# Kernel tuning notes

Hardware: AMD Instinct MI355X
Metric: run time of the kernel (lower is better)

The kernel has to match this reference:

```python
import jax, jax.numpy as jnp
import numpy as np

B, P, D_IN = 128, 4096, 4   # frames, points/frame, xyz+time
NG = 16                      # number of trajectory groups
H1, H2, H3 = 64, 128, 512    # PointNet shared-MLP widths


def _init_mlp(key, dims):
    ks = jax.random.split(key, len(dims) - 1)
    params = []
    for k, (di, do) in zip(ks, zip(dims[:-1], dims[1:])):
        W = jax.random.normal(k, (di, do), dtype=jnp.float32) * (1.0 / np.sqrt(di))
        b = jnp.zeros((do,), dtype=jnp.float32)
        params.append((W, b))
    return params


def setup_inputs() -> dict:
    key = jax.random.key(0)
    k_pc, k_t, k_idx, k_g, k_l = jax.random.split(key, 5)
    pc = jax.random.normal(k_pc, (B, 3, P), dtype=jnp.float32)
    traj_time_batch = jax.random.uniform(k_t, (B, 1), dtype=jnp.float32)
    traj_inbatch_index = jnp.sort(jax.random.randint(k_idx, (B,), 0, NG)).astype(jnp.int32)
    (Wg1, bg1), (Wg2, bg2), (Wg3, bg3) = _init_mlp(k_g, [D_IN, H1, H2, H3])
    (Wl1, bl1), (Wl2, bl2), (Wl3, bl3) = _init_mlp(k_l, [D_IN, H1, H2, H3])
    return dict(pc=pc, traj_time_batch=traj_time_batch, traj_inbatch_index=traj_inbatch_index,
                Wg1=Wg1, bg1=bg1, Wg2=Wg2, bg2=bg2, Wg3=Wg3, bg3=bg3,
                Wl1=Wl1, bl1=bl1, Wl2=Wl2, bl2=bl2, Wl3=Wl3, bl3=bl3)


def _mlp(x, layers):
    # pointwise shared MLP: x [..., P, d_in] -> [..., P, d_out]
    for W, b in layers:
        x = jax.nn.relu(x @ W + b)
    return x


def reference(pc, traj_time_batch, traj_inbatch_index,
              Wg1, bg1, Wg2, bg2, Wg3, bg3,
              Wl1, bl1, Wl2, bl2, Wl3, bl3):
    b, _, p = pc.shape
    # append time channel: [B,3,P] + [B,1,P] -> [B,4,P]
    t = jnp.broadcast_to(traj_time_batch[..., None], (b, 1, p))
    feat = jnp.concatenate([pc, t], axis=1)
    x = jnp.swapaxes(feat, 1, 2)  # [B,P,4] points-last layout for pointwise MLP

    # global branch: shared MLP on every point, then max over all points of each trajectory group
    hg = _mlp(x, [(Wg1, bg1), (Wg2, bg2), (Wg3, bg3)])           # [B,P,H3]
    seg = jnp.repeat(traj_inbatch_index, p)                       # [B*P]
    gmax = jax.ops.segment_max(hg.reshape(b * p, -1), seg, num_segments=NG)  # [NG,H3]
    global_feat = gmax[traj_inbatch_index]                        # [B,H3] broadcast back per frame

    # local branch: per-frame PointNet encode (shared MLP + max over points)
    hl = _mlp(x, [(Wl1, bl1), (Wl2, bl2), (Wl3, bl3)])            # [B,P,H3]
    local_feat = hl.max(axis=1)                                   # [B,H3]

    z = jnp.concatenate([global_feat, local_feat], axis=1)        # [B,2*H3]
    input_features_vis = pc                                       # original pc (last dim == 4096, no slice)
    return (z, input_features_vis)
```

## Files before the change

kernel.cpp:

```cpp
#include <hip/hip_runtime.h>
#include <hip/hip_bf16.h>

#define NB   128
#define NP   4096
#define NGRP 16
#define C3   512

typedef __bf16 bf16x8 __attribute__((ext_vector_type(8)));
typedef __bf16 bf16x4 __attribute__((ext_vector_type(4)));
typedef float  f32x4  __attribute__((ext_vector_type(4)));

#define WS_W1F_G 0
#define WS_W1F_L 4096
#define WS_W2F_G 8192
#define WS_W2F_L 24576
#define WS_W3F_G 40960
#define WS_W3F_L 172032
#define WS_GMAX  303104

__global__ __launch_bounds__(256) void prep_kernel(
    const float* __restrict__ Wg1, const float* __restrict__ Wg2, const float* __restrict__ Wg3,
    const float* __restrict__ Wl1, const float* __restrict__ Wl2, const float* __restrict__ Wl3,
    const float* __restrict__ pc, float* __restrict__ out, char* __restrict__ ws) {
    const int t = blockIdx.x, tid = threadIdx.x;
    if (t >= 37) {
        const f32x4* src = (const f32x4*)pc;
        f32x4* dst = (f32x4*)(out + NB * 2 * C3);
        int base = (t - 37) * 1024 + tid;
        #pragma unroll
        for (int j = 0; j < 4; ++j) dst[base + j * 256] = src[base + j * 256];
        return;
    }
    if (t == 36) {
        float* gmax = (float*)(ws + WS_GMAX);
        #pragma unroll
        for (int k = 0; k < 32; ++k) gmax[k * 256 + tid] = 0.0f;
        int c = tid >> 6, lane = tid & 63;
        int ch = c * 16 + (lane & 15);
        int kb = (lane >> 4) * 8;
        bf16x8 pg, pl;
        #pragma unroll
        for (int j = 0; j < 8; ++j) {
            int k = kb + j;
            pg[j] = (k < 4) ? (__bf16)Wg1[k * 64 + ch] : (__bf16)0.0f;
            pl[j] = (k < 4) ? (__bf16)Wl1[k * 64 + ch] : (__bf16)0.0f;
        }
        *(bf16x8*)((__bf16*)(ws + WS_W1F_G) + c * 512 + lane * 8) = pg;
        *(bf16x8*)((__bf16*)(ws + WS_W1F_L) + c * 512 + lane * 8) = pl;
        return;
    }
    __shared__ float tile[64][65];
    const float* src; __bf16* dst; int cBase, mMul, srcStride;
    if (t < 32) {
        int branch = t >> 4, rem = t & 15;
        int tk = rem >> 3, tc = rem & 7;
        src = (branch ? Wl3 : Wg3) + (size_t)(tk * 64) * 512 + tc * 64;
        dst = (__bf16*)(ws + (branch ? WS_W3F_L : WS_W3F_G));
        cBase = tc * 16 + tk * 2; mMul = 4; srcStride = 512;
    } else {
        int u = t - 32; int branch = u >> 1, tc = u & 1;
        src = (branch ? Wl2 : Wg2) + tc * 64;
        dst = (__bf16*)(ws + (branch ? WS_W2F_L : WS_W2F_G));
        cBase = tc * 8; mMul = 2; srcStride = 128;
    }
    {
        int r0 = tid >> 6, cl = tid & 63;
        #pragma unroll
        for (int p = 0; p < 16; ++p)
            tile[p * 4 + r0][cl] = src[(size_t)(p * 4 + r0) * srcStride + cl];
    }
    __syncthreads();
    int lane = tid & 63, l15 = lane & 15, q = lane >> 4;
    #pragma unroll
    for (int cc = 0; cc < 2; ++cc) {
        int pair = (tid >> 6) * 2 + cc;
        int mi = pair >> 1, ks = pair & 1;
        bf16x8 pk;
        #pragma unroll
        for (int j = 0; j < 8; ++j) pk[j] = (__bf16)tile[ks * 32 + q * 8 + j][mi * 16 + l15];
        *(bf16x8*)(dst + (cBase + mi * mMul + ks) * 512 + lane * 8) = pk;
    }
}

__global__ __launch_bounds__(512, 2) void main_kernel(
    const float* __restrict__ pc, const float* __restrict__ tt, const int* __restrict__ idx,
    const float* __restrict__ bg1, const float* __restrict__ bg2, const float* __restrict__ bg3,
    const float* __restrict__ bl1, const float* __restrict__ bl2, const float* __restrict__ bl3,
    float* __restrict__ out, char* __restrict__ ws) {
    __shared__ __align__(16) char smem[102912];
    __bf16* h2f = (__bf16*)smem;
    __bf16* w2f = (__bf16*)(smem + 65536);
    __bf16* h1s = (__bf16*)(smem + 81920);
    float*  b2s = (float*)(smem + 102400);

    const int tid = threadIdx.x, lane = tid & 63, wave = tid >> 6;
    const int quad = lane >> 4, l15 = lane & 15;
    const int branch = blockIdx.y, frame = blockIdx.x;

    const __bf16* w1g = (const __bf16*)(ws + (branch ? WS_W1F_L : WS_W1F_G));
    const __bf16* w2g = (const __bf16*)(ws + (branch ? WS_W2F_L : WS_W2F_G));
    const __bf16* w3g = (const __bf16*)(ws + (branch ? WS_W3F_L : WS_W3F_G));
    const float* b1 = branch ? bl1 : bg1;
    const float* b2 = branch ? bl2 : bg2;
    const float* b3 = branch ? bl3 : bg3;

    for (int i = tid; i < 1024; i += 512) ((f32x4*)w2f)[i] = ((const f32x4*)w2g)[i];
    if (tid < 128) b2s[tid] = b2[tid];

    bf16x8 a1[4];
    #pragma unroll
    for (int mi = 0; mi < 4; ++mi) a1[mi] = *(const bf16x8*)(w1g + mi * 512 + lane * 8);
    bf16x8 aw[4][4];
    #pragma unroll
    for (int mi = 0; mi < 4; ++mi)
        #pragma unroll
        for (int ks = 0; ks < 4; ++ks)
            aw[mi][ks] = *(const bf16x8*)(w3g + (wave * 16 + mi * 4 + ks) * 512 + lane * 8);

    float b1r[4][4];
    #pragma unroll
    for (int mi = 0; mi < 4; ++mi)
        #pragma unroll
        for (int r = 0; r < 4; ++r) b1r[mi][r] = b1[mi * 16 + quad * 4 + r];

    const float tval = tt[frame];
    const f32x4 zf = {0.0f, 0.0f, 0.0f, 0.0f};
    f32x4 runmax[4];
    #pragma unroll
    for (int mi = 0; mi < 4; ++mi) runmax[mi] = (f32x4){-1e30f, -1e30f, -1e30f, -1e30f};

    const float* pcx = pc + (size_t)frame * 3 * NP;
    __bf16* hs = h1s + wave * 1280;
    const int pw = wave * 16 + l15;

    float xx = pcx[pw], xy = pcx[NP + pw], xz = pcx[2 * NP + pw];

    __syncthreads();

    {
        bf16x8 xb;
        #pragma unroll
        for (int j = 0; j < 8; ++j) xb[j] = (__bf16)0.0f;
        if (quad == 0) { xb[0] = (__bf16)xx; xb[1] = (__bf16)xy; xb[2] = (__bf16)xz; xb[3] = (__bf16)tval; }
        #pragma unroll
        for (int mi = 0; mi < 4; ++mi) {
            f32x4 c = __builtin_amdgcn_mfma_f32_16x16x32_bf16(a1[mi], xb, zf, 0, 0, 0);
            bf16x4 pk;
            #pragma unroll
            for (int r = 0; r < 4; ++r) pk[r] = (__bf16)fmaxf(c[r] + b1r[mi][r], 0.0f);
            *(bf16x4*)(hs + l15 * 80 + mi * 16 + quad * 4) = pk;
        }
        bf16x8 hbf0 = *(const bf16x8*)(hs + l15 * 80 + quad * 8);
        bf16x8 hbf1 = *(const bf16x8*)(hs + l15 * 80 + 32 + quad * 8);
        #pragma unroll
        for (int mi = 0; mi < 8; ++mi) {
            bf16x8 a20 = *(const bf16x8*)(w2f + (mi * 2) * 512 + lane * 8);
            bf16x8 a21 = *(const bf16x8*)(w2f + (mi * 2 + 1) * 512 + lane * 8);
            f32x4 c = __builtin_amdgcn_mfma_f32_16x16x32_bf16(a20, hbf0, zf, 0, 0, 0);
            c = __builtin_amdgcn_mfma_f32_16x16x32_bf16(a21, hbf1, c, 0, 0, 0);
            f32x4 bb = *(const f32x4*)(b2s + mi * 16 + quad * 4);
            bf16x4 pk;
            #pragma unroll
            for (int r = 0; r < 4; ++r) pk[r] = (__bf16)fmaxf(c[r] + bb[r], 0.0f);
            const int c0 = mi * 16 + quad * 4;
            *(bf16x4*)(h2f + ((wave * 4 + (c0 >> 5)) * 4 + ((c0 >> 3) & 3)) * 128 + l15 * 8 + (c0 & 7)) = pk;
        }
    }

    for (int m = 0; m < 32; ++m) {
        __syncthreads();
        const __bf16* hb = h2f + (m & 1) * 16384;
        __bf16* hbn = h2f + ((m + 1) & 1) * 16384;
        const bool more = (m < 31);
        float nx = 0.f, ny = 0.f, nz = 0.f;
        if (more) {
            const int p = (m + 1) * 128 + pw;
            nx = pcx[p]; ny = pcx[NP + p]; nz = pcx[2 * NP + p];
        }
        bf16x8 hbf0, hbf1;
        bf16x8 bh0[4], bh1[4];
        #pragma unroll
        for (int ks = 0; ks < 4; ++ks) bh0[ks] = *(const bf16x8*)(hb + ks * 512 + lane * 8);
        #pragma unroll
        for (int ni = 0; ni < 8; ++ni) {
            bf16x8* cur = (ni & 1) ? bh1 : bh0;
            bf16x8* nxt = (ni & 1) ? bh0 : bh1;
            if (ni < 7) {
                #pragma unroll
                for (int ks = 0; ks < 4; ++ks)
                    nxt[ks] = *(const bf16x8*)(hb + ((ni + 1) * 4 + ks) * 512 + lane * 8);
            }
            f32x4 acc[4];
            #pragma unroll
            for (int ks = 0; ks < 4; ++ks)
                #pragma unroll
                for (int mi = 0; mi < 4; ++mi)
                    acc[mi] = __builtin_amdgcn_mfma_f32_16x16x32_bf16(
                        aw[mi][ks], cur[ks], ks ? acc[mi] : zf, 0, 0, 0);
            #pragma unroll
            for (int mi = 0; mi < 4; ++mi)
                #pragma unroll
                for (int r = 0; r < 4; ++r)
                    runmax[mi][r] = fmaxf(runmax[mi][r], acc[mi][r]);

            if (more && ni == 2) {
                bf16x8 xb;
                #pragma unroll
                for (int j = 0; j < 8; ++j) xb[j] = (__bf16)0.0f;
                if (quad == 0) { xb[0] = (__bf16)nx; xb[1] = (__bf16)ny; xb[2] = (__bf16)nz; xb[3] = (__bf16)tval; }
                #pragma unroll
                for (int mi = 0; mi < 4; ++mi) {
                    f32x4 c = __builtin_amdgcn_mfma_f32_16x16x32_bf16(a1[mi], xb, zf, 0, 0, 0);
                    bf16x4 pk;
                    #pragma unroll
                    for (int r = 0; r < 4; ++r) pk[r] = (__bf16)fmaxf(c[r] + b1r[mi][r], 0.0f);
                    *(bf16x4*)(hs + l15 * 80 + mi * 16 + quad * 4) = pk;
                }
            }
            if (more && ni == 4) {
                hbf0 = *(const bf16x8*)(hs + l15 * 80 + quad * 8);
                hbf1 = *(const bf16x8*)(hs + l15 * 80 + 32 + quad * 8);
            }
            if (more && ni == 6) {
                #pragma unroll
                for (int mi = 0; mi < 8; ++mi) {
                    bf16x8 a20 = *(const bf16x8*)(w2f + (mi * 2) * 512 + lane * 8);
                    bf16x8 a21 = *(const bf16x8*)(w2f + (mi * 2 + 1) * 512 + lane * 8);
                    f32x4 c = __builtin_amdgcn_mfma_f32_16x16x32_bf16(a20, hbf0, zf, 0, 0, 0);
                    c = __builtin_amdgcn_mfma_f32_16x16x32_bf16(a21, hbf1, c, 0, 0, 0);
                    f32x4 bb = *(const f32x4*)(b2s + mi * 16 + quad * 4);
                    bf16x4 pk;
                    #pragma unroll
                    for (int r = 0; r < 4; ++r) pk[r] = (__bf16)fmaxf(c[r] + bb[r], 0.0f);
                    const int c0 = mi * 16 + quad * 4;
                    *(bf16x4*)(hbn + ((wave * 4 + (c0 >> 5)) * 4 + ((c0 >> 3) & 3)) * 128 + l15 * 8 + (c0 & 7)) = pk;
                }
            }
        }
    }

    const int g = idx[frame];
    float* gmax = (float*)(ws + WS_GMAX);
    #pragma unroll
    for (int mi = 0; mi < 4; ++mi) {
        f32x4 v = runmax[mi];
        #pragma unroll
        for (int d = 1; d < 16; d <<= 1) {
            #pragma unroll
            for (int r = 0; r < 4; ++r) v[r] = fmaxf(v[r], __shfl_xor(v[r], d));
        }
        if (l15 == 0) {
            #pragma unroll
            for (int r = 0; r < 4; ++r) {
                const int ch = wave * 64 + mi * 16 + quad * 4 + r;
                const float fv = fmaxf(v[r] + b3[ch], 0.0f);
                if (branch == 0)
                    atomicMax((unsigned*)(gmax + g * C3 + ch), __float_as_uint(fv));
                else
                    out[(size_t)frame * (2 * C3) + C3 + ch] = fv;
            }
        }
    }
}

__global__ void gather_kernel(const int* __restrict__ idx, const char* __restrict__ ws,
                              float* __restrict__ out) {
    int i = blockIdx.x * blockDim.x + threadIdx.x;
    int b = i >> 9, ch = i & 511;
    const float* gmax = (const float*)(ws + WS_GMAX);
    out[b * (2 * C3) + ch] = gmax[idx[b] * C3 + ch];
}

extern "C" void kernel_launch(void* const* d_in, const int* in_sizes, int n_in,
                              void* d_out, int out_size, void* d_ws, size_t ws_size,
                              hipStream_t stream) {
    const float* pc  = (const float*)d_in[0];
    const float* tt  = (const float*)d_in[1];
    const int*   idx = (const int*)d_in[2];
    const float* Wg1 = (const float*)d_in[3];  const float* bg1 = (const float*)d_in[4];
    const float* Wg2 = (const float*)d_in[5];  const float* bg2 = (const float*)d_in[6];
    const float* Wg3 = (const float*)d_in[7];  const float* bg3 = (const float*)d_in[8];
    const float* Wl1 = (const float*)d_in[9];  const float* bl1 = (const float*)d_in[10];
    const float* Wl2 = (const float*)d_in[11]; const float* bl2 = (const float*)d_in[12];
    const float* Wl3 = (const float*)d_in[13]; const float* bl3 = (const float*)d_in[14];
    float* out = (float*)d_out;
    char*  ws  = (char*)d_ws;

    prep_kernel<<<421, 256, 0, stream>>>(Wg1, Wg2, Wg3, Wl1, Wl2, Wl3, pc, out, ws);
    main_kernel<<<dim3(128, 2), 512, 0, stream>>>(pc, tt, idx, bg1, bg2, bg3,
                                                  bl1, bl2, bl3, out, ws);
    gather_kernel<<<256, 256, 0, stream>>>(idx, ws, out);
}
```

Baseline: 202.7 us.

## Split each frame's points across two blocks and single-buffer the layer-2 tile

Launches 512 blocks instead of 256 by splitting each frame's 4096 points into two halves. The local branch now merges the halves with atomicMax into an output pre-zeroed in prep. The double-buffered h2 tile becomes one buffer with an extra barrier, which cuts shared memory so more blocks fit per CU, and launch bounds are raised to 4 blocks. The pc copy moves from prep into the gather kernel. In exchange the layer-2 compute is no longer overlapped with layer-3, there is an extra sync per iteration, and register pressure rises from the tighter launch bounds.

```diff
diff --git a/kernel.cpp b/kernel.cpp
--- a/kernel.cpp
+++ b/kernel.cpp
@@ -23,12 +23,14 @@
     const float* __restrict__ Wl1, const float* __restrict__ Wl2, const float* __restrict__ Wl3,
     const float* __restrict__ pc, float* __restrict__ out, char* __restrict__ ws) {
     const int t = blockIdx.x, tid = threadIdx.x;
+    (void)pc;
     if (t >= 37) {
-        const f32x4* src = (const f32x4*)pc;
-        f32x4* dst = (f32x4*)(out + NB * 2 * C3);
-        int base = (t - 37) * 1024 + tid;
-        #pragma unroll
-        for (int j = 0; j < 4; ++j) dst[base + j * 256] = src[base + j * 256];
+        int base = (t - 37) * 8192 + tid;
+        #pragma unroll
+        for (int k = 0; k < 32; ++k) {
+            int i = base + k * 256;
+            out[(i >> 9) * (2 * C3) + C3 + (i & 511)] = 0.0f;
+        }
         return;
     }
     if (t == 36) {
@@ -82,20 +84,20 @@
     }
 }
 
-__global__ __launch_bounds__(512, 2) void main_kernel(
+__global__ __launch_bounds__(512, 4) void main_kernel(
     const float* __restrict__ pc, const float* __restrict__ tt, const int* __restrict__ idx,
     const float* __restrict__ bg1, const float* __restrict__ bg2, const float* __restrict__ bg3,
     const float* __restrict__ bl1, const float* __restrict__ bl2, const float* __restrict__ bl3,
     float* __restrict__ out, char* __restrict__ ws) {
-    __shared__ __align__(16) char smem[102912];
+    __shared__ __align__(16) char smem[70144];
     __bf16* h2f = (__bf16*)smem;
-    __bf16* w2f = (__bf16*)(smem + 65536);
-    __bf16* h1s = (__bf16*)(smem + 81920);
-    float*  b2s = (float*)(smem + 102400);
+    __bf16* w2f = (__bf16*)(smem + 32768);
+    __bf16* h1s = (__bf16*)(smem + 49152);
+    float*  b2s = (float*)(smem + 69632);
 
     const int tid = threadIdx.x, lane = tid & 63, wave = tid >> 6;
     const int quad = lane >> 4, l15 = lane & 15;
-    const int branch = blockIdx.y, frame = blockIdx.x;
+    const int branch = blockIdx.y, frame = blockIdx.x, hblk = blockIdx.z;
 
     const __bf16* w1g = (const __bf16*)(ws + (branch ? WS_W1F_L : WS_W1F_G));
     const __bf16* w2g = (const __bf16*)(ws + (branch ? WS_W2F_L : WS_W2F_G));
@@ -132,8 +134,9 @@
     const float* pcx = pc + (size_t)frame * 3 * NP;
     __bf16* hs = h1s + wave * 1280;
     const int pw = wave * 16 + l15;
-
-    float xx = pcx[pw], xy = pcx[NP + pw], xz = pcx[2 * NP + pw];
+    const int pbase = hblk * 2048;
+
+    float xx = pcx[pbase + pw], xy = pcx[NP + pbase + pw], xz = pcx[2 * NP + pbase + pw];
 
     __syncthreads();
 
@@ -167,20 +170,18 @@
         }
     }
 
-    for (int m = 0; m < 32; ++m) {
+    for (int m = 0; m < 16; ++m) {
         __syncthreads();
-        const __bf16* hb = h2f + (m & 1) * 16384;
-        __bf16* hbn = h2f + ((m + 1) & 1) * 16384;
-        const bool more = (m < 31);
+        const bool more = (m < 15);
         float nx = 0.f, ny = 0.f, nz = 0.f;
         if (more) {
-            const int p = (m + 1) * 128 + pw;
+            const int p = pbase + (m + 1) * 128 + pw;
             nx = pcx[p]; ny = pcx[NP + p]; nz = pcx[2 * NP + p];
         }
         bf16x8 hbf0, hbf1;
         bf16x8 bh0[4], bh1[4];
         #pragma unroll
-        for (int ks = 0; ks < 4; ++ks) bh0[ks] = *(const bf16x8*)(hb + ks * 512 + lane * 8);
+        for (int ks = 0; ks < 4; ++ks) bh0[ks] = *(const bf16x8*)(h2f + ks * 512 + lane * 8);
         #pragma unroll
         for (int ni = 0; ni < 8; ++ni) {
             bf16x8* cur = (ni & 1) ? bh1 : bh0;
@@ -188,7 +189,7 @@
             if (ni < 7) {
                 #pragma unroll
                 for (int ks = 0; ks < 4; ++ks)
-                    nxt[ks] = *(const bf16x8*)(hb + ((ni + 1) * 4 + ks) * 512 + lane * 8);
+                    nxt[ks] = *(const bf16x8*)(h2f + ((ni + 1) * 4 + ks) * 512 + lane * 8);
             }
             f32x4 acc[4];
             #pragma unroll
@@ -221,20 +222,21 @@
                 hbf0 = *(const bf16x8*)(hs + l15 * 80 + quad * 8);
                 hbf1 = *(const bf16x8*)(hs + l15 * 80 + 32 + quad * 8);
             }
-            if (more && ni == 6) {
-                #pragma unroll
-                for (int mi = 0; mi < 8; ++mi) {
-                    bf16x8 a20 = *(const bf16x8*)(w2f + (mi * 2) * 512 + lane * 8);
-                    bf16x8 a21 = *(const bf16x8*)(w2f + (mi * 2 + 1) * 512 + lane * 8);
-                    f32x4 c = __builtin_amdgcn_mfma_f32_16x16x32_bf16(a20, hbf0, zf, 0, 0, 0);
-                    c = __builtin_amdgcn_mfma_f32_16x16x32_bf16(a21, hbf1, c, 0, 0, 0);
-                    f32x4 bb = *(const f32x4*)(b2s + mi * 16 + quad * 4);
-                    bf16x4 pk;
-                    #pragma unroll
-                    for (int r = 0; r < 4; ++r) pk[r] = (__bf16)fmaxf(c[r] + bb[r], 0.0f);
-                    const int c0 = mi * 16 + quad * 4;
-                    *(bf16x4*)(hbn + ((wave * 4 + (c0 >> 5)) * 4 + ((c0 >> 3) & 3)) * 128 + l15 * 8 + (c0 & 7)) = pk;
-                }
+        }
+        __syncthreads();
+        if (more) {
+            #pragma unroll
+            for (int mi = 0; mi < 8; ++mi) {
+                bf16x8 a20 = *(const bf16x8*)(w2f + (mi * 2) * 512 + lane * 8);
+                bf16x8 a21 = *(const bf16x8*)(w2f + (mi * 2 + 1) * 512 + lane * 8);
+                f32x4 c = __builtin_amdgcn_mfma_f32_16x16x32_bf16(a20, hbf0, zf, 0, 0, 0);
+                c = __builtin_amdgcn_mfma_f32_16x16x32_bf16(a21, hbf1, c, 0, 0, 0);
+                f32x4 bb = *(const f32x4*)(b2s + mi * 16 + quad * 4);
+                bf16x4 pk;
+                #pragma unroll
+                for (int r = 0; r < 4; ++r) pk[r] = (__bf16)fmaxf(c[r] + bb[r], 0.0f);
+                const int c0 = mi * 16 + quad * 4;
+                *(bf16x4*)(h2f + ((wave * 4 + (c0 >> 5)) * 4 + ((c0 >> 3) & 3)) * 128 + l15 * 8 + (c0 & 7)) = pk;
             }
         }
     }
@@ -257,18 +259,23 @@
                 if (branch == 0)
                     atomicMax((unsigned*)(gmax + g * C3 + ch), __float_as_uint(fv));
                 else
-                    out[(size_t)frame * (2 * C3) + C3 + ch] = fv;
+                    atomicMax((unsigned*)(out + (size_t)frame * (2 * C3) + C3 + ch),
+                              __float_as_uint(fv));
             }
         }
     }
 }
 
 __global__ void gather_kernel(const int* __restrict__ idx, const char* __restrict__ ws,
-                              float* __restrict__ out) {
+                              const float* __restrict__ pc, float* __restrict__ out) {
     int i = blockIdx.x * blockDim.x + threadIdx.x;
     int b = i >> 9, ch = i & 511;
     const float* gmax = (const float*)(ws + WS_GMAX);
     out[b * (2 * C3) + ch] = gmax[idx[b] * C3 + ch];
+    const f32x4* src = (const f32x4*)pc;
+    f32x4* dst = (f32x4*)(out + NB * 2 * C3);
+    #pragma unroll
+    for (int j = 0; j < 6; ++j) dst[i + j * 65536] = src[i + j * 65536];
 }
 
 extern "C" void kernel_launch(void* const* d_in, const int* in_sizes, int n_in,
@@ -286,8 +293,8 @@
     float* out = (float*)d_out;
     char*  ws  = (char*)d_ws;
 
-    prep_kernel<<<421, 256, 0, stream>>>(Wg1, Wg2, Wg3, Wl1, Wl2, Wl3, pc, out, ws);
-    main_kernel<<<dim3(128, 2), 512, 0, stream>>>(pc, tt, idx, bg1, bg2, bg3,
-                                                  bl1, bl2, bl3, out, ws);
-    gather_kernel<<<256, 256, 0, stream>>>(idx, ws, out);
+    prep_kernel<<<45, 256, 0, stream>>>(Wg1, Wg2, Wg3, Wl1, Wl2, Wl3, pc, out, ws);
+    main_kernel<<<dim3(128, 2, 2), 512, 0, stream>>>(pc, tt, idx, bg1, bg2, bg3,
+                                                     bl1, bl2, bl3, out, ws);
+    gather_kernel<<<256, 256, 0, stream>>>(idx, ws, pc, out);
 }
```

Measured after the change: 788.1 us. +288.8%, slower.

## Keep W2 fragments in registers, stagger layer-1/2 per wave, move pc copy

Applied to the files above, without the earlier changes.

Layer-2 weight fragments are now loaded once into registers instead of staged in LDS and re-read every iteration, which shrinks the LDS footprint and removes LDS traffic. The layer-1/2 recompute slots are staggered between the two halves of the waves so they do not all leave the MFMA pipe at once. The layer-3 MFMA block runs at raised wave priority. The pc passthrough copy moves from the prep kernel into the gather kernel, shortening the prep launch. The cost is 16 extra VGPR vectors per thread under a 2-block occupancy bound, which risks spills.

```diff
diff --git a/kernel.cpp b/kernel.cpp
--- a/kernel.cpp
+++ b/kernel.cpp
@@ -21,16 +21,8 @@
 __global__ __launch_bounds__(256) void prep_kernel(
     const float* __restrict__ Wg1, const float* __restrict__ Wg2, const float* __restrict__ Wg3,
     const float* __restrict__ Wl1, const float* __restrict__ Wl2, const float* __restrict__ Wl3,
-    const float* __restrict__ pc, float* __restrict__ out, char* __restrict__ ws) {
+    char* __restrict__ ws) {
     const int t = blockIdx.x, tid = threadIdx.x;
-    if (t >= 37) {
-        const f32x4* src = (const f32x4*)pc;
-        f32x4* dst = (f32x4*)(out + NB * 2 * C3);
-        int base = (t - 37) * 1024 + tid;
-        #pragma unroll
-        for (int j = 0; j < 4; ++j) dst[base + j * 256] = src[base + j * 256];
-        return;
-    }
     if (t == 36) {
         float* gmax = (float*)(ws + WS_GMAX);
         #pragma unroll
@@ -87,11 +79,10 @@
     const float* __restrict__ bg1, const float* __restrict__ bg2, const float* __restrict__ bg3,
     const float* __restrict__ bl1, const float* __restrict__ bl2, const float* __restrict__ bl3,
     float* __restrict__ out, char* __restrict__ ws) {
-    __shared__ __align__(16) char smem[102912];
+    __shared__ __align__(16) char smem[86528];
     __bf16* h2f = (__bf16*)smem;
-    __bf16* w2f = (__bf16*)(smem + 65536);
-    __bf16* h1s = (__bf16*)(smem + 81920);
-    float*  b2s = (float*)(smem + 102400);
+    __bf16* h1s = (__bf16*)(smem + 65536);
+    float*  b2s = (float*)(smem + 86016);
 
     const int tid = threadIdx.x, lane = tid & 63, wave = tid >> 6;
     const int quad = lane >> 4, l15 = lane & 15;
@@ -104,12 +95,14 @@
     const float* b2 = branch ? bl2 : bg2;
     const float* b3 = branch ? bl3 : bg3;
 
-    for (int i = tid; i < 1024; i += 512) ((f32x4*)w2f)[i] = ((const f32x4*)w2g)[i];
     if (tid < 128) b2s[tid] = b2[tid];
 
     bf16x8 a1[4];
     #pragma unroll
     for (int mi = 0; mi < 4; ++mi) a1[mi] = *(const bf16x8*)(w1g + mi * 512 + lane * 8);
+    bf16x8 a2[16];
+    #pragma unroll
+    for (int c = 0; c < 16; ++c) a2[c] = *(const bf16x8*)(w2g + c * 512 + lane * 8);
     bf16x8 aw[4][4];
     #pragma unroll
     for (int mi = 0; mi < 4; ++mi)
@@ -132,6 +125,9 @@
     const float* pcx = pc + (size_t)frame * 3 * NP;
     __bf16* hs = h1s + wave * 1280;
     const int pw = wave * 16 + l15;
+    const int sA = 2 + (wave >> 2);
+    const int sB = sA + 2;
+    const int sC = sA + 4;
 
     float xx = pcx[pw], xy = pcx[NP + pw], xz = pcx[2 * NP + pw];
 
@@ -154,10 +150,8 @@
         bf16x8 hbf1 = *(const bf16x8*)(hs + l15 * 80 + 32 + quad * 8);
         #pragma unroll
         for (int mi = 0; mi < 8; ++mi) {
-            bf16x8 a20 = *(const bf16x8*)(w2f + (mi * 2) * 512 + lane * 8);
-            bf16x8 a21 = *(const bf16x8*)(w2f + (mi * 2 + 1) * 512 + lane * 8);
-            f32x4 c = __builtin_amdgcn_mfma_f32_16x16x32_bf16(a20, hbf0, zf, 0, 0, 0);
-            c = __builtin_amdgcn_mfma_f32_16x16x32_bf16(a21, hbf1, c, 0, 0, 0);
+            f32x4 c = __builtin_amdgcn_mfma_f32_16x16x32_bf16(a2[mi * 2], hbf0, zf, 0, 0, 0);
+            c = __builtin_amdgcn_mfma_f32_16x16x32_bf16(a2[mi * 2 + 1], hbf1, c, 0, 0, 0);
             f32x4 bb = *(const f32x4*)(b2s + mi * 16 + quad * 4);
             bf16x4 pk;
             #pragma unroll
@@ -191,19 +185,21 @@
                     nxt[ks] = *(const bf16x8*)(hb + ((ni + 1) * 4 + ks) * 512 + lane * 8);
             }
             f32x4 acc[4];
+            __builtin_amdgcn_s_setprio(1);
             #pragma unroll
             for (int ks = 0; ks < 4; ++ks)
                 #pragma unroll
                 for (int mi = 0; mi < 4; ++mi)
                     acc[mi] = __builtin_amdgcn_mfma_f32_16x16x32_bf16(
                         aw[mi][ks], cur[ks], ks ? acc[mi] : zf, 0, 0, 0);
+            __builtin_amdgcn_s_setprio(0);
             #pragma unroll
             for (int mi = 0; mi < 4; ++mi)
                 #pragma unroll
                 for (int r = 0; r < 4; ++r)
                     runmax[mi][r] = fmaxf(runmax[mi][r], acc[mi][r]);
 
-            if (more && ni == 2) {
+            if (more && ni == sA) {
                 bf16x8 xb;
                 #pragma unroll
                 for (int j = 0; j < 8; ++j) xb[j] = (__bf16)0.0f;
@@ -217,17 +213,15 @@
                     *(bf16x4*)(hs + l15 * 80 + mi * 16 + quad * 4) = pk;
                 }
             }
-            if (more && ni == 4) {
+            if (more && ni == sB) {
                 hbf0 = *(const bf16x8*)(hs + l15 * 80 + quad * 8);
                 hbf1 = *(const bf16x8*)(hs + l15 * 80 + 32 + quad * 8);
             }
-            if (more && ni == 6) {
+            if (more && ni == sC) {
                 #pragma unroll
                 for (int mi = 0; mi < 8; ++mi) {
-                    bf16x8 a20 = *(const bf16x8*)(w2f + (mi * 2) * 512 + lane * 8);
-                    bf16x8 a21 = *(const bf16x8*)(w2f + (mi * 2 + 1) * 512 + lane * 8);
-                    f32x4 c = __builtin_amdgcn_mfma_f32_16x16x32_bf16(a20, hbf0, zf, 0, 0, 0);
-                    c = __builtin_amdgcn_mfma_f32_16x16x32_bf16(a21, hbf1, c, 0, 0, 0);
+                    f32x4 c = __builtin_amdgcn_mfma_f32_16x16x32_bf16(a2[mi * 2], hbf0, zf, 0, 0, 0);
+                    c = __builtin_amdgcn_mfma_f32_16x16x32_bf16(a2[mi * 2 + 1], hbf1, c, 0, 0, 0);
                     f32x4 bb = *(const f32x4*)(b2s + mi * 16 + quad * 4);
                     bf16x4 pk;
                     #pragma unroll
@@ -264,11 +258,15 @@
 }
 
 __global__ void gather_kernel(const int* __restrict__ idx, const char* __restrict__ ws,
-                              float* __restrict__ out) {
+                              const float* __restrict__ pc, float* __restrict__ out) {
     int i = blockIdx.x * blockDim.x + threadIdx.x;
     int b = i >> 9, ch = i & 511;
     const float* gmax = (const float*)(ws + WS_GMAX);
     out[b * (2 * C3) + ch] = gmax[idx[b] * C3 + ch];
+    const f32x4* src = (const f32x4*)pc;
+    f32x4* dst = (f32x4*)(out + NB * 2 * C3);
+    #pragma unroll
+    for (int j = 0; j < 6; ++j) dst[i + j * 65536] = src[i + j * 65536];
 }
 
 extern "C" void kernel_launch(void* const* d_in, const int* in_sizes, int n_in,
@@ -286,8 +284,8 @@
     float* out = (float*)d_out;
     char*  ws  = (char*)d_ws;
 
-    prep_kernel<<<421, 256, 0, stream>>>(Wg1, Wg2, Wg3, Wl1, Wl2, Wl3, pc, out, ws);
+    prep_kernel<<<37, 256, 0, stream>>>(Wg1, Wg2, Wg3, Wl1, Wl2, Wl3, ws);
     main_kernel<<<dim3(128, 2), 512, 0, stream>>>(pc, tt, idx, bg1, bg2, bg3,
                                                   bl1, bl2, bl3, out, ws);
-    gather_kernel<<<256, 256, 0, stream>>>(idx, ws, out);
-}
+    gather_kernel<<<256, 256, 0, stream>>>(idx, ws, pc, out);
+}
```

Result: slower. 378.1 us (+86.5%).

## Stagger layer-1/2 work across wave halves, add MFMA priority, move pc copy

Applied to the files above, without the earlier changes.

Moves the main GEMM loop body into a templated helper. The two halves of the waves now run their interleaved layer-1/layer-2 work at different MFMA steps, with s_setprio raised around each layer-3 MFMA burst, so the LDS/VALU phases of different waves overlap with the MFMA phases. The h1 scratch row stride shrinks from 80 to 72 elements, which reduces shared memory use. The pc passthrough copy moves from prep_kernel into gather_kernel so the prep launch has fewer blocks. These changes rely on schedule effects that may not hold; the copy now runs serially after the main kernel rather than in the prep step.

```diff
diff --git a/kernel.cpp b/kernel.cpp
--- a/kernel.cpp
+++ b/kernel.cpp
@@ -21,16 +21,8 @@
 __global__ __launch_bounds__(256) void prep_kernel(
     const float* __restrict__ Wg1, const float* __restrict__ Wg2, const float* __restrict__ Wg3,
     const float* __restrict__ Wl1, const float* __restrict__ Wl2, const float* __restrict__ Wl3,
-    const float* __restrict__ pc, float* __restrict__ out, char* __restrict__ ws) {
+    char* __restrict__ ws) {
     const int t = blockIdx.x, tid = threadIdx.x;
-    if (t >= 37) {
-        const f32x4* src = (const f32x4*)pc;
-        f32x4* dst = (f32x4*)(out + NB * 2 * C3);
-        int base = (t - 37) * 1024 + tid;
-        #pragma unroll
-        for (int j = 0; j < 4; ++j) dst[base + j * 256] = src[base + j * 256];
-        return;
-    }
     if (t == 36) {
         float* gmax = (float*)(ws + WS_GMAX);
         #pragma unroll
@@ -82,16 +74,90 @@
     }
 }
 
+template<int SA>
+__device__ __forceinline__ void macro_body(
+    const __bf16* __restrict__ hb, __bf16* __restrict__ hbn,
+    const __bf16* __restrict__ w2f, const float* __restrict__ b2s,
+    __bf16* __restrict__ hs, const bf16x8 (&aw)[4][4], const bf16x8 (&a1)[4],
+    const float (&b1r)[4][4], f32x4 (&runmax)[4],
+    float nx, float ny, float nz, float tval,
+    int lane, int quad, int l15, int wave, bool more) {
+    constexpr int SB = SA + 2, SC = SA + 4;
+    const f32x4 zf = {0.0f, 0.0f, 0.0f, 0.0f};
+    bf16x8 hbf0, hbf1;
+    bf16x8 bh0[4], bh1[4];
+    #pragma unroll
+    for (int ks = 0; ks < 4; ++ks) bh0[ks] = *(const bf16x8*)(hb + ks * 512 + lane * 8);
+    #pragma unroll
+    for (int ni = 0; ni < 8; ++ni) {
+        bf16x8* cur = (ni & 1) ? bh1 : bh0;
+        bf16x8* nxt = (ni & 1) ? bh0 : bh1;
+        if (ni < 7) {
+            #pragma unroll
+            for (int ks = 0; ks < 4; ++ks)
+                nxt[ks] = *(const bf16x8*)(hb + ((ni + 1) * 4 + ks) * 512 + lane * 8);
+        }
+        f32x4 acc[4];
+        __builtin_amdgcn_s_setprio(1);
+        #pragma unroll
+        for (int ks = 0; ks < 4; ++ks)
+            #pragma unroll
+            for (int mi = 0; mi < 4; ++mi)
+                acc[mi] = __builtin_amdgcn_mfma_f32_16x16x32_bf16(
+                    aw[mi][ks], cur[ks], ks ? acc[mi] : zf, 0, 0, 0);
+        __builtin_amdgcn_s_setprio(0);
+        #pragma unroll
+        for (int mi = 0; mi < 4; ++mi)
+            #pragma unroll
+            for (int r = 0; r < 4; ++r)
+                runmax[mi][r] = fmaxf(runmax[mi][r], acc[mi][r]);
+
+        if (more && ni == SA) {
+            bf16x8 xb;
+            #pragma unroll
+            for (int j = 0; j < 8; ++j) xb[j] = (__bf16)0.0f;
+            if (quad == 0) { xb[0] = (__bf16)nx; xb[1] = (__bf16)ny; xb[2] = (__bf16)nz; xb[3] = (__bf16)tval; }
+            #pragma unroll
+            for (int mi = 0; mi < 4; ++mi) {
+                f32x4 c = __builtin_amdgcn_mfma_f32_16x16x32_bf16(a1[mi], xb, zf, 0, 0, 0);
+                bf16x4 pk;
+                #pragma unroll
+                for (int r = 0; r < 4; ++r) pk[r] = (__bf16)fmaxf(c[r] + b1r[mi][r], 0.0f);
+                *(bf16x4*)(hs + l15 * 72 + mi * 16 + quad * 4) = pk;
+            }
+        }
+        if (more && ni == SB) {
+            hbf0 = *(const bf16x8*)(hs + l15 * 72 + quad * 8);
+            hbf1 = *(const bf16x8*)(hs + l15 * 72 + 32 + quad * 8);
+        }
+        if (more && ni == SC) {
+            #pragma unroll
+            for (int mi = 0; mi < 8; ++mi) {
+                bf16x8 a20 = *(const bf16x8*)(w2f + (mi * 2) * 512 + lane * 8);
+                bf16x8 a21 = *(const bf16x8*)(w2f + (mi * 2 + 1) * 512 + lane * 8);
+                f32x4 c = __builtin_amdgcn_mfma_f32_16x16x32_bf16(a20, hbf0, zf, 0, 0, 0);
+                c = __builtin_amdgcn_mfma_f32_16x16x32_bf16(a21, hbf1, c, 0, 0, 0);
+                f32x4 bb = *(const f32x4*)(b2s + mi * 16 + quad * 4);
+                bf16x4 pk;
+                #pragma unroll
+                for (int r = 0; r < 4; ++r) pk[r] = (__bf16)fmaxf(c[r] + bb[r], 0.0f);
+                const int c0 = mi * 16 + quad * 4;
+                *(bf16x4*)(hbn + ((wave * 4 + (c0 >> 5)) * 4 + ((c0 >> 3) & 3)) * 128 + l15 * 8 + (c0 & 7)) = pk;
+            }
+        }
+    }
+}
+
 __global__ __launch_bounds__(512, 2) void main_kernel(
     const float* __restrict__ pc, const float* __restrict__ tt, const int* __restrict__ idx,
     const float* __restrict__ bg1, const float* __restrict__ bg2, const float* __restrict__ bg3,
     const float* __restrict__ bl1, const float* __restrict__ bl2, const float* __restrict__ bl3,
     float* __restrict__ out, char* __restrict__ ws) {
-    __shared__ __align__(16) char smem[102912];
+    __shared__ __align__(16) char smem[100864];
     __bf16* h2f = (__bf16*)smem;
     __bf16* w2f = (__bf16*)(smem + 65536);
     __bf16* h1s = (__bf16*)(smem + 81920);
-    float*  b2s = (float*)(smem + 102400);
+    float*  b2s = (float*)(smem + 100352);
 
     const int tid = threadIdx.x, lane = tid & 63, wave = tid >> 6;
     const int quad = lane >> 4, l15 = lane & 15;
@@ -130,7 +196,7 @@
     for (int mi = 0; mi < 4; ++mi) runmax[mi] = (f32x4){-1e30f, -1e30f, -1e30f, -1e30f};
 
     const float* pcx = pc + (size_t)frame * 3 * NP;
-    __bf16* hs = h1s + wave * 1280;
+    __bf16* hs = h1s + wave * 1152;
     const int pw = wave * 16 + l15;
 
     float xx = pcx[pw], xy = pcx[NP + pw], xz = pcx[2 * NP + pw];
@@ -148,10 +214,10 @@
             bf16x4 pk;
             #pragma unroll
             for (int r = 0; r < 4; ++r) pk[r] = (__bf16)fmaxf(c[r] + b1r[mi][r], 0.0f);
-            *(bf16x4*)(hs + l15 * 80 + mi * 16 + quad * 4) = pk;
-        }
-        bf16x8 hbf0 = *(const bf16x8*)(hs + l15 * 80 + quad * 8);
-        bf16x8 hbf1 = *(const bf16x8*)(hs + l15 * 80 + 32 + quad * 8);
+            *(bf16x4*)(hs + l15 * 72 + mi * 16 + quad * 4) = pk;
+        }
+        bf16x8 hbf0 = *(const bf16x8*)(hs + l15 * 72 + quad * 8);
+        bf16x8 hbf1 = *(const bf16x8*)(hs + l15 * 72 + 32 + quad * 8);
         #pragma unroll
         for (int mi = 0; mi < 8; ++mi) {
             bf16x8 a20 = *(const bf16x8*)(w2f + (mi * 2) * 512 + lane * 8);
@@ -177,66 +243,12 @@
             const int p = (m + 1) * 128 + pw;
             nx = pcx[p]; ny = pcx[NP + p]; nz = pcx[2 * NP + p];
         }
-        bf16x8 hbf0, hbf1;
-        bf16x8 bh0[4], bh1[4];
-        #pragma unroll
-        for (int ks = 0; ks < 4; ++ks) bh0[ks] = *(const bf16x8*)(hb + ks * 512 + lane * 8);
-        #pragma unroll
-        for (int ni = 0; ni < 8; ++ni) {
-            bf16x8* cur = (ni & 1) ? bh1 : bh0;
-            bf16x8* nxt = (ni & 1) ? bh0 : bh1;
-            if (ni < 7) {
-                #pragma unroll
-                for (int ks = 0; ks < 4; ++ks)
-                    nxt[ks] = *(const bf16x8*)(hb + ((ni + 1) * 4 + ks) * 512 + lane * 8);
-            }
-            f32x4 acc[4];
-            #pragma unroll
-            for (int ks = 0; ks < 4; ++ks)
-                #pragma unroll
-                for (int mi = 0; mi < 4; ++mi)
-                    acc[mi] = __builtin_amdgcn_mfma_f32_16x16x32_bf16(
-                        aw[mi][ks], cur[ks], ks ? acc[mi] : zf, 0, 0, 0);
-            #pragma unroll
-            for (int mi = 0; mi < 4; ++mi)
-                #pragma unroll
-                for (int r = 0; r < 4; ++r)
-                    runmax[mi][r] = fmaxf(runmax[mi][r], acc[mi][r]);
-
-            if (more && ni == 2) {
-                bf16x8 xb;
-                #pragma unroll
-                for (int j = 0; j < 8; ++j) xb[j] = (__bf16)0.0f;
-                if (quad == 0) { xb[0] = (__bf16)nx; xb[1] = (__bf16)ny; xb[2] = (__bf16)nz; xb[3] = (__bf16)tval; }
-                #pragma unroll
-                for (int mi = 0; mi < 4; ++mi) {
-                    f32x4 c = __builtin_amdgcn_mfma_f32_16x16x32_bf16(a1[mi], xb, zf, 0, 0, 0);
-                    bf16x4 pk;
-                    #pragma unroll
-                    for (int r = 0; r < 4; ++r) pk[r] = (__bf16)fmaxf(c[r] + b1r[mi][r], 0.0f);
-                    *(bf16x4*)(hs + l15 * 80 + mi * 16 + quad * 4) = pk;
-                }
-            }
-            if (more && ni == 4) {
-                hbf0 = *(const bf16x8*)(hs + l15 * 80 + quad * 8);
-                hbf1 = *(const bf16x8*)(hs + l15 * 80 + 32 + quad * 8);
-            }
-            if (more && ni == 6) {
-                #pragma unroll
-                for (int mi = 0; mi < 8; ++mi) {
-                    bf16x8 a20 = *(const bf16x8*)(w2f + (mi * 2) * 512 + lane * 8);
-                    bf16x8 a21 = *(const bf16x8*)(w2f + (mi * 2 + 1) * 512 + lane * 8);
-                    f32x4 c = __builtin_amdgcn_mfma_f32_16x16x32_bf16(a20, hbf0, zf, 0, 0, 0);
-                    c = __builtin_amdgcn_mfma_f32_16x16x32_bf16(a21, hbf1, c, 0, 0, 0);
-                    f32x4 bb = *(const f32x4*)(b2s + mi * 16 + quad * 4);
-                    bf16x4 pk;
-                    #pragma unroll
-                    for (int r = 0; r < 4; ++r) pk[r] = (__bf16)fmaxf(c[r] + bb[r], 0.0f);
-                    const int c0 = mi * 16 + quad * 4;
-                    *(bf16x4*)(hbn + ((wave * 4 + (c0 >> 5)) * 4 + ((c0 >> 3) & 3)) * 128 + l15 * 8 + (c0 & 7)) = pk;
-                }
-            }
-        }
+        if ((wave & 4) == 0)
+            macro_body<2>(hb, hbn, w2f, b2s, hs, aw, a1, b1r, runmax,
+                          nx, ny, nz, tval, lane, quad, l15, wave, more);
+        else
+            macro_body<3>(hb, hbn, w2f, b2s, hs, aw, a1, b1r, runmax,
+                          nx, ny, nz, tval, lane, quad, l15, wave, more);
     }
 
     const int g = idx[frame];
@@ -264,11 +276,15 @@
 }
 
 __global__ void gather_kernel(const int* __restrict__ idx, const char* __restrict__ ws,
-                              float* __restrict__ out) {
+                              const float* __restrict__ pc, float* __restrict__ out) {
     int i = blockIdx.x * blockDim.x + threadIdx.x;
     int b = i >> 9, ch = i & 511;
     const float* gmax = (const float*)(ws + WS_GMAX);
     out[b * (2 * C3) + ch] = gmax[idx[b] * C3 + ch];
+    const f32x4* src = (const f32x4*)pc;
+    f32x4* dst = (f32x4*)(out + NB * 2 * C3);
+    #pragma unroll
+    for (int j = 0; j < 6; ++j) dst[i + j * 65536] = src[i + j * 65536];
 }
 
 extern "C" void kernel_launch(void* const* d_in, const int* in_sizes, int n_in,
@@ -286,8 +302,8 @@
     float* out = (float*)d_out;
     char*  ws  = (char*)d_ws;
 
-    prep_kernel<<<421, 256, 0, stream>>>(Wg1, Wg2, Wg3, Wl1, Wl2, Wl3, pc, out, ws);
+    prep_kernel<<<37, 256, 0, stream>>>(Wg1, Wg2, Wg3, Wl1, Wl2, Wl3, ws);
     main_kernel<<<dim3(128, 2), 512, 0, stream>>>(pc, tt, idx, bg1, bg2, bg3,
                                                   bl1, bl2, bl3, out, ws);
-    gather_kernel<<<256, 256, 0, stream>>>(idx, ws, out);
-}
+    gather_kernel<<<256, 256, 0, stream>>>(idx, ws, pc, out);
+}
```

Measured after the change: 226.1 us. 11.5% more time.
